# Performance work log

Hardware: AMD Instinct MI355X
Metric: run time of the kernel (lower is better)

The kernel has to match this reference:

```python
import jax, jax.numpy as jnp
import numpy as np

D_MODEL = 768
NUM_HEADS = 12
D_K = D_MODEL // NUM_HEADS
SCALE = float(np.sqrt(D_K))


def setup_inputs() -> dict:
    key = jax.random.key(0)
    ks = jax.random.split(key, 9)
    B, S, D = 2, 2048, D_MODEL
    std = 1.0 / np.sqrt(D)
    x = jax.random.normal(ks[0], (B, S, D), dtype=jnp.float32)
    attention_mask = jnp.ones((B, S), dtype=jnp.int32)
    # Linear params: weight [out, in] (torch convention), bias [out]
    Wq = jax.random.normal(ks[1], (D, D), dtype=jnp.float32) * std
    bq = jax.random.normal(ks[2], (D,), dtype=jnp.float32) * 0.01
    Wk = jax.random.normal(ks[3], (D, D), dtype=jnp.float32) * std
    bk = jax.random.normal(ks[4], (D,), dtype=jnp.float32) * 0.01
    Wv = jax.random.normal(ks[5], (D, D), dtype=jnp.float32) * std
    bv = jax.random.normal(ks[6], (D,), dtype=jnp.float32) * 0.01
    Wo = jax.random.normal(ks[7], (D, D), dtype=jnp.float32) * std
    bo = jax.random.normal(ks[8], (D,), dtype=jnp.float32) * 0.01
    return {"x": x, "attention_mask": attention_mask,
            "Wq": Wq, "bq": bq, "Wk": Wk, "bk": bk,
            "Wv": Wv, "bv": bv, "Wo": Wo, "bo": bo}


def reference(x, attention_mask, Wq, bq, Wk, bk, Wv, bv, Wo, bo):
    B, S, D = x.shape
    H, Dk = NUM_HEADS, D_K
    # QKV projections (torch Linear: x @ W.T + b)
    q = (x @ Wq.T + bq).reshape(B, S, H, Dk).transpose(0, 2, 1, 3)  # [B,H,S,Dk]
    k = (x @ Wk.T + bk).reshape(B, S, H, Dk).transpose(0, 2, 1, 3)
    v = (x @ Wv.T + bv).reshape(B, S, H, Dk).transpose(0, 2, 1, 3)
    scores = jnp.einsum('bhqd,bhkd->bhqk', q, k) / SCALE  # [B,H,S,S]
    mask = attention_mask[:, None, None, :]  # [B,1,1,S]
    scores = jnp.where(mask == 0, jnp.float32(-jnp.inf), scores)
    attn = jax.nn.softmax(scores, axis=-1)
    # dropout is identity in eval mode
    ctx = jnp.einsum('bhqk,bhkd->bhqd', attn, v)  # [B,H,S,Dk]
    ctx = ctx.transpose(0, 2, 1, 3).reshape(B, S, D)
    return ctx @ Wo.T + bo
```

## Files before the change

kernel.cpp:

```cpp
#include <hip/hip_runtime.h>
#include <stdint.h>

#define NHEAD 12
#define DKH   64
#define BB    2
#define SS    2048
#define DMOD  768
#define MTOT  (BB*SS)
#define NCHUNK 4
#define CHS   (SS/NCHUNK)
#define QBLK  128
#define NT    (CHS/64)

typedef __attribute__((ext_vector_type(8)))  _Float16 half8;
typedef __attribute__((ext_vector_type(4)))  _Float16 half4;
typedef __attribute__((ext_vector_type(2)))  __fp16   fp16x2;
typedef __attribute__((ext_vector_type(4)))  float    f32x4;
typedef __attribute__((ext_vector_type(16))) float    f32x16;

typedef __attribute__((address_space(1))) const void gv_t;
typedef __attribute__((address_space(3))) void       lv_t;

__device__ inline float fexp2(float x) { return __builtin_amdgcn_exp2f(x); }
__device__ inline int pk2(float a, float b) {
    union { fp16x2 h; int i; } u;
    u.h = __builtin_amdgcn_cvt_pkrtz(a, b);
    return u.i;
}

__global__ void k_cvt(const float* __restrict__ in, _Float16* __restrict__ out, int n) {
    int i = (blockIdx.x * 256 + threadIdx.x) * 4;
    if (i >= n) return;
    float4 v = *(const float4*)(in + i);
    half4 o;
    o.x = (_Float16)v.x; o.y = (_Float16)v.y; o.z = (_Float16)v.z; o.w = (_Float16)v.w;
    *(half4*)(out + i) = o;
}

__global__ void k_cvtw(const float* __restrict__ w0, const float* __restrict__ w1,
                       const float* __restrict__ w2, const float* __restrict__ w3,
                       _Float16* __restrict__ o0, _Float16* __restrict__ o1,
                       _Float16* __restrict__ o2, _Float16* __restrict__ o3) {
    const float* in; _Float16* out;
    switch (blockIdx.y) {
        case 0: in = w0; out = o0; break;
        case 1: in = w1; out = o1; break;
        case 2: in = w2; out = o2; break;
        default: in = w3; out = o3; break;
    }
    int i = (blockIdx.x * 256 + threadIdx.x) * 4;
    float4 v = *(const float4*)(in + i);
    half4 o;
    o.x = (_Float16)v.x; o.y = (_Float16)v.y; o.z = (_Float16)v.z; o.w = (_Float16)v.w;
    *(half4*)(out + i) = o;
}

template<int MODE>
__global__ __launch_bounds__(256, 2) void k_gemm(
    const _Float16* __restrict__ A, const _Float16* __restrict__ Bm,
    const float* __restrict__ bias0, const float* __restrict__ bias1, const float* __restrict__ bias2,
    float* __restrict__ outF,
    _Float16* __restrict__ Qd, _Float16* __restrict__ Kd, _Float16* __restrict__ Vtd,
    int K, int Ncols)
{
    __shared__ _Float16 As[128 * 64];
    __shared__ _Float16 Bs[128 * 64];
    const int tid = threadIdx.x;
    const int w = tid >> 6, l = tid & 63, lr = l & 15, lg = l >> 4;
    const int bm = blockIdx.y * 128, bn = blockIdx.x * 128;
    const int wm = (w >> 1) * 64, wn = (w & 1) * 64;
    f32x4 acc[4][4] = {};

    for (int k0 = 0; k0 < K; k0 += 64) {
        __syncthreads();
#pragma unroll
        for (int i = 0; i < 4; ++i) {
            int o  = w * 4096 + i * 1024 + l * 16;
            int lo = o ^ (((o >> 7) & 7) << 4);
            int row = lo >> 7;
            int colb = lo & 127;
            __builtin_amdgcn_global_load_lds(
                (gv_t*)((const char*)A + ((size_t)(bm + row) * K + k0) * 2 + colb),
                (lv_t*)((char*)As + w * 4096 + i * 1024), 16, 0, 0);
            __builtin_amdgcn_global_load_lds(
                (gv_t*)((const char*)Bm + ((size_t)(bn + row) * K + k0) * 2 + colb),
                (lv_t*)((char*)Bs + w * 4096 + i * 1024), 16, 0, 0);
        }
        __syncthreads();
#pragma unroll
        for (int kk = 0; kk < 2; ++kk) {
            half8 af[4], bf[4];
#pragma unroll
            for (int f = 0; f < 4; ++f) {
                int ob = ((wm + f * 16 + lr) * 128 + kk * 64 + lg * 16) ^ ((lr & 7) << 4);
                af[f] = *(const half8*)((const char*)As + ob);
                int ob2 = ((wn + f * 16 + lr) * 128 + kk * 64 + lg * 16) ^ ((lr & 7) << 4);
                bf[f] = *(const half8*)((const char*)Bs + ob2);
            }
            __builtin_amdgcn_s_setprio(1);
#pragma unroll
            for (int fm = 0; fm < 4; ++fm)
#pragma unroll
                for (int fn = 0; fn < 4; ++fn)
                    acc[fm][fn] = __builtin_amdgcn_mfma_f32_16x16x32_f16(af[fm], bf[fn], acc[fm][fn], 0, 0, 0);
            __builtin_amdgcn_s_setprio(0);
        }
    }

#pragma unroll
    for (int fm = 0; fm < 4; ++fm) {
#pragma unroll
        for (int fn = 0; fn < 4; ++fn) {
            int n = bn + wn + fn * 16 + lr;
            if (MODE == 0) {
                float bia = bias0[n];
#pragma unroll
                for (int j = 0; j < 4; ++j) {
                    int m = bm + wm + fm * 16 + lg * 4 + j;
                    outF[(size_t)m * Ncols + n] = acc[fm][fn][j] + bia;
                }
            } else {
                int qkv = n / 768, nn = n - qkv * 768;
                const float* bp = (qkv == 0) ? bias0 : (qkv == 1 ? bias1 : bias2);
                float bia = bp[nn];
                int h = nn >> 6, dk = nn & 63;
                int m0 = bm + wm + fm * 16 + lg * 4;
                int b = m0 >> 11;
                int s0 = m0 & 2047;
                size_t head = (size_t)b * NHEAD + h;
                if (qkv == 2) {
                    half4 pk;
#pragma unroll
                    for (int j = 0; j < 4; ++j) pk[j] = (_Float16)(acc[fm][fn][j] + bia);
                    *(half4*)(Vtd + (head * DKH + dk) * SS + s0) = pk;
                } else {
                    _Float16* dst = (qkv == 0) ? Qd : Kd;
                    float qsc = (qkv == 0) ? 0.18033688011f : 1.0f;
#pragma unroll
                    for (int j = 0; j < 4; ++j)
                        dst[(head * SS + (s0 + j)) * DKH + dk] = (_Float16)((acc[fm][fn][j] + bia) * qsc);
                }
            }
        }
    }
}

__global__ __launch_bounds__(256, 3) void k_attn(
    const _Float16* __restrict__ Qd, const _Float16* __restrict__ Kd,
    const _Float16* __restrict__ Vtd, const int* __restrict__ mask,
    _Float16* __restrict__ Opart, float* __restrict__ Mpart, float* __restrict__ Lpart)
{
    __shared__ _Float16 Ks[2 * 64 * 64];
    __shared__ _Float16 Vs[2 * 64 * 64];
    const int tid = threadIdx.x, w = tid >> 6, l = tid & 63;
    const int lq = l & 31, lhi = l >> 5;
    const int F = blockIdx.x;
    const int gid = (F & 7) * 192 + (F >> 3);
    const int head  = gid >> 6;
    const int rem   = gid & 63;
    const int qt    = rem >> 2;
    const int chunk = rem & 3;
    const int b = head / NHEAD;
    const char* Qh = (const char*)(Qd + (size_t)head * SS * DKH);
    const char* Kh = (const char*)(Kd + (size_t)head * SS * DKH) + (size_t)chunk * CHS * 128;
    const char* Vh = (const char*)(Vtd + (size_t)head * DKH * SS);
    const int vcb = chunk * CHS * 2;

    const int q = qt * QBLK + w * 32 + lq;
    half8 qf[4];
#pragma unroll
    for (int kd = 0; kd < 4; ++kd)
        qf[kd] = *(const half8*)(Qh + ((size_t)q * 64 + kd * 16 + lhi * 8) * 2);

    f32x16 accO[2] = {};
    f32x16 sumA = {};
    float m = -__builtin_inff();
    half8 onesv;
#pragma unroll
    for (int i = 0; i < 8; ++i) onesv[i] = (_Float16)1.0f;

    auto STAGE = [&](int kt2, int buf) {
#pragma unroll
        for (int i = 0; i < 2; ++i) {
            int o  = w * 2048 + i * 1024 + l * 16;
            int lo = o ^ (((o >> 7) & 7) << 4);
            __builtin_amdgcn_global_load_lds(
                (gv_t*)(Kh + (size_t)kt2 * 8192 + lo),
                (lv_t*)((char*)Ks + buf * 8192 + w * 2048 + i * 1024), 16, 0, 0);
            int dv = lo >> 7, inner = lo & 127;
            __builtin_amdgcn_global_load_lds(
                (gv_t*)(Vh + (size_t)dv * 4096 + vcb + kt2 * 128 + inner),
                (lv_t*)((char*)Vs + buf * 8192 + w * 2048 + i * 1024), 16, 0, 0);
        }
    };

    STAGE(0, 0);
    int cur = 0;

    for (int kt = 0; kt < NT; ++kt) {
        __syncthreads();
        if (kt < NT - 1) STAGE(kt + 1, cur ^ 1);
        int mv = mask[b * SS + chunk * CHS + kt * 64 + l];
        unsigned long long bal = __ballot(mv != 0);
        const char* kb = (const char*)Ks + cur * 8192;
        const char* vb = (const char*)Vs + cur * 8192;

        f32x16 s0 = {}, s1 = {};
        __builtin_amdgcn_s_setprio(1);
#pragma unroll
        for (int kd = 0; kd < 4; ++kd) {
            int col = kd * 32 + lhi * 16;
            int ob0 = (lq * 128 + col) ^ ((lq & 7) << 4);
            half8 kf0 = *(const half8*)(kb + ob0);
            s0 = __builtin_amdgcn_mfma_f32_32x32x16_f16(kf0, qf[kd], s0, 0, 0, 0);
            int ob1 = ((32 + lq) * 128 + col) ^ ((lq & 7) << 4);
            half8 kf1 = *(const half8*)(kb + ob1);
            s1 = __builtin_amdgcn_mfma_f32_32x32x16_f16(kf1, qf[kd], s1, 0, 0, 0);
        }
        __builtin_amdgcn_s_setprio(0);

        if (bal != ~0ull) {
#pragma unroll
            for (int r = 0; r < 16; ++r) {
                int kv0 = (r & 3) + 8 * (r >> 2) + 4 * lhi;
                if (!((bal >> kv0) & 1))        s0[r] = -__builtin_inff();
                if (!((bal >> (kv0 + 32)) & 1)) s1[r] = -__builtin_inff();
            }
        }

        float t[16];
#pragma unroll
        for (int i = 0; i < 16; ++i) t[i] = fmaxf(s0[i], s1[i]);
#pragma unroll
        for (int i = 0; i < 8; ++i) t[i] = fmaxf(t[i], t[i + 8]);
#pragma unroll
        for (int i = 0; i < 4; ++i) t[i] = fmaxf(t[i], t[i + 4]);
        t[0] = fmaxf(fmaxf(t[0], t[2]), fmaxf(t[1], t[3]));
        float pmax = fmaxf(t[0], __shfl_xor(t[0], 32, 64));

        if (!__all(pmax <= m + 3.0f)) {
            float mnew = fmaxf(m, pmax);
            float f = fexp2(m - mnew);
            m = mnew;
            accO[0] *= f; accO[1] *= f; sumA *= f;
        }
        float mex = fmaxf(m, -1e30f);

#pragma unroll
        for (int i = 0; i < 16; ++i) { s0[i] = fexp2(s0[i] - mex); s1[i] = fexp2(s1[i] - mex); }

        union PF { int w[4]; half8 h; } pf[4];
        {
            int W[8];
#pragma unroll
            for (int mm = 0; mm < 8; ++mm) W[mm] = pk2(s0[2 * mm], s0[2 * mm + 1]);
            asm("v_permlane32_swap_b32 %0, %1" : "+v"(W[0]), "+v"(W[2]));
            asm("v_permlane32_swap_b32 %0, %1" : "+v"(W[1]), "+v"(W[3]));
            asm("v_permlane32_swap_b32 %0, %1" : "+v"(W[4]), "+v"(W[6]));
            asm("v_permlane32_swap_b32 %0, %1" : "+v"(W[5]), "+v"(W[7]));
            pf[0].w[0] = W[0]; pf[0].w[1] = W[1]; pf[0].w[2] = W[2]; pf[0].w[3] = W[3];
            pf[1].w[0] = W[4]; pf[1].w[1] = W[5]; pf[1].w[2] = W[6]; pf[1].w[3] = W[7];
#pragma unroll
            for (int mm = 0; mm < 8; ++mm) W[mm] = pk2(s1[2 * mm], s1[2 * mm + 1]);
            asm("v_permlane32_swap_b32 %0, %1" : "+v"(W[0]), "+v"(W[2]));
            asm("v_permlane32_swap_b32 %0, %1" : "+v"(W[1]), "+v"(W[3]));
            asm("v_permlane32_swap_b32 %0, %1" : "+v"(W[4]), "+v"(W[6]));
            asm("v_permlane32_swap_b32 %0, %1" : "+v"(W[5]), "+v"(W[7]));
            pf[2].w[0] = W[0]; pf[2].w[1] = W[1]; pf[2].w[2] = W[2]; pf[2].w[3] = W[3];
            pf[3].w[0] = W[4]; pf[3].w[1] = W[5]; pf[3].w[2] = W[6]; pf[3].w[3] = W[7];
        }

        __builtin_amdgcn_s_setprio(1);
#pragma unroll
        for (int cc = 0; cc < 4; ++cc) {
            int col = cc * 32 + lhi * 16;
#pragma unroll
            for (int ds = 0; ds < 2; ++ds) {
                int vrow = ds * 32 + lq;
                int ob = (vrow * 128 + col) ^ ((lq & 7) << 4);
                half8 vf = *(const half8*)(vb + ob);
                accO[ds] = __builtin_amdgcn_mfma_f32_32x32x16_f16(vf, pf[cc].h, accO[ds], 0, 0, 0);
            }
            sumA = __builtin_amdgcn_mfma_f32_32x32x16_f16(onesv, pf[cc].h, sumA, 0, 0, 0);
        }
        __builtin_amdgcn_s_setprio(0);
        cur ^= 1;
    }

    const size_t prow = (size_t)(chunk * BB * NHEAD + head) * SS;
    if (lhi == 0) { Mpart[prow + q] = m; Lpart[prow + q] = sumA[0]; }
#pragma unroll
    for (int ds = 0; ds < 2; ++ds)
#pragma unroll
        for (int rq = 0; rq < 4; ++rq) {
            half4 hv;
#pragma unroll
            for (int j = 0; j < 4; ++j) hv[j] = (_Float16)accO[ds][rq * 4 + j];
            *(half4*)(Opart + (prow + q) * DKH + ds * 32 + rq * 8 + lhi * 4) = hv;
        }
}

__global__ __launch_bounds__(256) void k_merge(
    const _Float16* __restrict__ Opart, const float* __restrict__ Mpart,
    const float* __restrict__ Lpart, _Float16* __restrict__ Ctx)
{
    int row  = blockIdx.x * 4 + (threadIdx.x >> 6);
    int lane = threadIdx.x & 63;
    int head = row >> 11, q = row & 2047;
    int b = head / NHEAD, h = head - b * NHEAD;
    float m[NCHUNK], lv[NCHUNK], M = -__builtin_inff();
#pragma unroll
    for (int c = 0; c < NCHUNK; ++c) {
        size_t pr = (size_t)(c * BB * NHEAD + head) * SS + q;
        m[c] = Mpart[pr]; lv[c] = Lpart[pr];
        M = fmaxf(M, m[c]);
    }
    float outv = 0.f;
    if (M > -1e37f) {
        float L = 0.f, acc = 0.f;
#pragma unroll
        for (int c = 0; c < NCHUNK; ++c) {
            float wgt = fexp2(m[c] - M);
            L += lv[c] * wgt;
            acc += wgt * (float)Opart[((size_t)(c * BB * NHEAD + head) * SS + q) * DKH + lane];
        }
        outv = acc / L;
    }
    Ctx[((size_t)(b * SS) + q) * DMOD + h * DKH + lane] = (_Float16)outv;
}

extern "C" void kernel_launch(void* const* d_in, const int* in_sizes, int n_in,
                              void* d_out, int out_size, void* d_ws, size_t ws_size,
                              hipStream_t stream) {
    const float* x  = (const float*)d_in[0];
    const int*  msk = (const int*)d_in[1];
    const float* Wq = (const float*)d_in[2];
    const float* bq = (const float*)d_in[3];
    const float* Wk = (const float*)d_in[4];
    const float* bk = (const float*)d_in[5];
    const float* Wv = (const float*)d_in[6];
    const float* bv = (const float*)d_in[7];
    const float* Wo = (const float*)d_in[8];
    const float* bo = (const float*)d_in[9];

    char* ws = (char*)d_ws;
    _Float16* Xb   = (_Float16*)(ws);
    _Float16* Wqkv = (_Float16*)(ws + 6291456);
    _Float16* Wob  = (_Float16*)(ws + 9830400);
    _Float16* Qd   = (_Float16*)(ws + 11010048);
    _Float16* Kd   = (_Float16*)(ws + 17301504);
    _Float16* Vtd  = (_Float16*)(ws + 23592960);
    _Float16* Ctxb = (_Float16*)(ws + 29884416);
    _Float16* Opart= (_Float16*)(ws + 36175872);
    float*    Mpart= (float*)   (ws + 61341696);
    float*    Lpart= (float*)   (ws + 62128128);

    k_cvt<<<3072, 256, 0, stream>>>(x, Xb, MTOT * DMOD);
    k_cvtw<<<dim3(576, 4), 256, 0, stream>>>(Wq, Wk, Wv, Wo,
                                             Wqkv, Wqkv + 589824, Wqkv + 1179648, Wob);

    k_gemm<1><<<dim3(18, 32), 256, 0, stream>>>(Xb, Wqkv, bq, bk, bv,
                                                nullptr, Qd, Kd, Vtd, DMOD, 0);
    k_attn<<<dim3(24 * 16 * NCHUNK), 256, 0, stream>>>(Qd, Kd, Vtd, msk, Opart, Mpart, Lpart);
    k_merge<<<12288, 256, 0, stream>>>(Opart, Mpart, Lpart, Ctxb);
    k_gemm<0><<<dim3(6, 32), 256, 0, stream>>>(Ctxb, Wob, bo, nullptr, nullptr,
                                               (float*)d_out, nullptr, nullptr, nullptr,
                                               DMOD, DMOD);
}
```

Before: 117.3 us.

## Double attention query block per workgroup, fuse conversion kernels, stage output through LDS

Raises the attention query block from 128 to 256 rows, using 512-thread workgroups, so each staged K/V tile in LDS is shared by eight waves instead of four. This halves global K/V traffic per query and halves the block count. The epilogue now writes the partial output through swizzled LDS and stores coalesced 16-byte rows instead of scattered half4 writes. The two fp32-to-fp16 conversion kernels become one launch. The trade-off is fewer workgroups (768) and lower occupancy per CU, with extra barriers in the epilogue.

Result: faster. 113.1 us (-3.6%).

```diff
diff --git a/kernel.cpp b/kernel.cpp
--- a/kernel.cpp
+++ b/kernel.cpp
@@ -9,7 +9,7 @@
 #define MTOT  (BB*SS)
 #define NCHUNK 4
 #define CHS   (SS/NCHUNK)
-#define QBLK  128
+#define QBLK  256
 #define NT    (CHS/64)
 
 typedef __attribute__((ext_vector_type(8)))  _Float16 half8;
@@ -28,27 +28,20 @@
     return u.i;
 }
 
-__global__ void k_cvt(const float* __restrict__ in, _Float16* __restrict__ out, int n) {
-    int i = (blockIdx.x * 256 + threadIdx.x) * 4;
-    if (i >= n) return;
-    float4 v = *(const float4*)(in + i);
-    half4 o;
-    o.x = (_Float16)v.x; o.y = (_Float16)v.y; o.z = (_Float16)v.z; o.w = (_Float16)v.w;
-    *(half4*)(out + i) = o;
-}
-
-__global__ void k_cvtw(const float* __restrict__ w0, const float* __restrict__ w1,
-                       const float* __restrict__ w2, const float* __restrict__ w3,
-                       _Float16* __restrict__ o0, _Float16* __restrict__ o1,
-                       _Float16* __restrict__ o2, _Float16* __restrict__ o3) {
-    const float* in; _Float16* out;
-    switch (blockIdx.y) {
-        case 0: in = w0; out = o0; break;
-        case 1: in = w1; out = o1; break;
-        case 2: in = w2; out = o2; break;
-        default: in = w3; out = o3; break;
-    }
-    int i = (blockIdx.x * 256 + threadIdx.x) * 4;
+__global__ void k_cvtall(const float* __restrict__ x,
+                         const float* __restrict__ w0, const float* __restrict__ w1,
+                         const float* __restrict__ w2, const float* __restrict__ w3,
+                         _Float16* __restrict__ xb,
+                         _Float16* __restrict__ o0, _Float16* __restrict__ o1,
+                         _Float16* __restrict__ o2, _Float16* __restrict__ o3) {
+    const float* in; _Float16* out; int base;
+    int blk = blockIdx.x;
+    if (blk < 3072)      { in = x;  out = xb; base = blk; }
+    else if (blk < 3648) { in = w0; out = o0; base = blk - 3072; }
+    else if (blk < 4224) { in = w1; out = o1; base = blk - 3648; }
+    else if (blk < 4800) { in = w2; out = o2; base = blk - 4224; }
+    else                 { in = w3; out = o3; base = blk - 4800; }
+    int i = (base * 256 + threadIdx.x) * 4;
     float4 v = *(const float4*)(in + i);
     half4 o;
     o.x = (_Float16)v.x; o.y = (_Float16)v.y; o.z = (_Float16)v.z; o.w = (_Float16)v.w;
@@ -145,19 +138,18 @@
     }
 }
 
-__global__ __launch_bounds__(256, 3) void k_attn(
+__global__ __launch_bounds__(512, 2) void k_attn(
     const _Float16* __restrict__ Qd, const _Float16* __restrict__ Kd,
     const _Float16* __restrict__ Vtd, const int* __restrict__ mask,
     _Float16* __restrict__ Opart, float* __restrict__ Mpart, float* __restrict__ Lpart)
 {
-    __shared__ _Float16 Ks[2 * 64 * 64];
-    __shared__ _Float16 Vs[2 * 64 * 64];
+    __shared__ _Float16 SM[16384];
     const int tid = threadIdx.x, w = tid >> 6, l = tid & 63;
     const int lq = l & 31, lhi = l >> 5;
     const int F = blockIdx.x;
-    const int gid = (F & 7) * 192 + (F >> 3);
-    const int head  = gid >> 6;
-    const int rem   = gid & 63;
+    const int gid = (F & 7) * 96 + (F >> 3);
+    const int head  = gid >> 5;
+    const int rem   = gid & 31;
     const int qt    = rem >> 2;
     const int chunk = rem & 3;
     const int b = head / NHEAD;
@@ -180,18 +172,15 @@
     for (int i = 0; i < 8; ++i) onesv[i] = (_Float16)1.0f;
 
     auto STAGE = [&](int kt2, int buf) {
-#pragma unroll
-        for (int i = 0; i < 2; ++i) {
-            int o  = w * 2048 + i * 1024 + l * 16;
-            int lo = o ^ (((o >> 7) & 7) << 4);
-            __builtin_amdgcn_global_load_lds(
-                (gv_t*)(Kh + (size_t)kt2 * 8192 + lo),
-                (lv_t*)((char*)Ks + buf * 8192 + w * 2048 + i * 1024), 16, 0, 0);
-            int dv = lo >> 7, inner = lo & 127;
-            __builtin_amdgcn_global_load_lds(
-                (gv_t*)(Vh + (size_t)dv * 4096 + vcb + kt2 * 128 + inner),
-                (lv_t*)((char*)Vs + buf * 8192 + w * 2048 + i * 1024), 16, 0, 0);
-        }
+        int o  = tid * 16;
+        int lo = o ^ (((o >> 7) & 7) << 4);
+        __builtin_amdgcn_global_load_lds(
+            (gv_t*)(Kh + (size_t)kt2 * 8192 + lo),
+            (lv_t*)((char*)SM + buf * 8192 + o), 16, 0, 0);
+        int dv = lo >> 7, inner = lo & 127;
+        __builtin_amdgcn_global_load_lds(
+            (gv_t*)(Vh + (size_t)dv * 4096 + vcb + kt2 * 128 + inner),
+            (lv_t*)((char*)SM + 16384 + buf * 8192 + o), 16, 0, 0);
     };
 
     STAGE(0, 0);
@@ -202,8 +191,8 @@
         if (kt < NT - 1) STAGE(kt + 1, cur ^ 1);
         int mv = mask[b * SS + chunk * CHS + kt * 64 + l];
         unsigned long long bal = __ballot(mv != 0);
-        const char* kb = (const char*)Ks + cur * 8192;
-        const char* vb = (const char*)Vs + cur * 8192;
+        const char* kb = (const char*)SM + cur * 8192;
+        const char* vb = (const char*)SM + 16384 + cur * 8192;
 
         f32x16 s0 = {}, s1 = {};
         __builtin_amdgcn_s_setprio(1);
@@ -289,15 +278,27 @@
 
     const size_t prow = (size_t)(chunk * BB * NHEAD + head) * SS;
     if (lhi == 0) { Mpart[prow + q] = m; Lpart[prow + q] = sumA[0]; }
+    __syncthreads();
+    char* ep = (char*)SM;
+    const int qrow = w * 32 + lq;
 #pragma unroll
     for (int ds = 0; ds < 2; ++ds)
 #pragma unroll
-        for (int rq = 0; rq < 4; ++rq) {
-            half4 hv;
-#pragma unroll
-            for (int j = 0; j < 4; ++j) hv[j] = (_Float16)accO[ds][rq * 4 + j];
-            *(half4*)(Opart + (prow + q) * DKH + ds * 32 + rq * 8 + lhi * 4) = hv;
-        }
+        for (int r = 0; r < 16; ++r) {
+            int dv = ds * 32 + (r & 3) + 8 * (r >> 2) + 4 * lhi;
+            int ad = (qrow * 128 + dv * 2) ^ ((qrow & 7) << 4);
+            *(_Float16*)(ep + ad) = (_Float16)accO[ds][r];
+        }
+    __syncthreads();
+    const size_t obase = prow + qt * QBLK;
+#pragma unroll
+    for (int i = 0; i < 4; ++i) {
+        int c16 = i * 512 + tid;
+        int qr = c16 >> 3, c8 = c16 & 7;
+        int la = (qr * 128 + c8 * 16) ^ ((qr & 7) << 4);
+        half8 v = *(const half8*)(ep + la);
+        *(half8*)(Opart + (obase + qr) * DKH + c8 * 8) = v;
+    }
 }
 
 __global__ __launch_bounds__(256) void k_merge(
@@ -355,13 +356,12 @@
     float*    Mpart= (float*)   (ws + 61341696);
     float*    Lpart= (float*)   (ws + 62128128);
 
-    k_cvt<<<3072, 256, 0, stream>>>(x, Xb, MTOT * DMOD);
-    k_cvtw<<<dim3(576, 4), 256, 0, stream>>>(Wq, Wk, Wv, Wo,
-                                             Wqkv, Wqkv + 589824, Wqkv + 1179648, Wob);
+    k_cvtall<<<5376, 256, 0, stream>>>(x, Wq, Wk, Wv, Wo,
+                                       Xb, Wqkv, Wqkv + 589824, Wqkv + 1179648, Wob);
 
     k_gemm<1><<<dim3(18, 32), 256, 0, stream>>>(Xb, Wqkv, bq, bk, bv,
                                                 nullptr, Qd, Kd, Vtd, DMOD, 0);
-    k_attn<<<dim3(24 * 16 * NCHUNK), 256, 0, stream>>>(Qd, Kd, Vtd, msk, Opart, Mpart, Lpart);
+    k_attn<<<dim3(24 * (SS / QBLK) * NCHUNK), 512, 0, stream>>>(Qd, Kd, Vtd, msk, Opart, Mpart, Lpart);
     k_merge<<<12288, 256, 0, stream>>>(Opart, Mpart, Lpart, Ctxb);
     k_gemm<0><<<dim3(6, 32), 256, 0, stream>>>(Ctxb, Wob, bo, nullptr, nullptr,
                                                (float*)d_out, nullptr, nullptr, nullptr,
```
